# Performance work log

Measured on AMD Instinct MI355X. Metric: run time of the kernel, lower is better.

The kernel has to match this reference:

```python
import jax, jax.numpy as jnp
import numpy as np

EMBED = 2048
MLP = 8192
EPS = 1e-5


def setup_inputs() -> dict:
    key = jax.random.key(0)
    ks = jax.random.split(key, 16)
    s = 0.02
    inp = {
        "x": jax.random.normal(ks[0], (2, 2048, EMBED), dtype=jnp.float32),
        "wq": jax.random.normal(ks[1], (EMBED, EMBED), dtype=jnp.float32) * s,
        "bq": jnp.zeros((EMBED,), jnp.float32),
        "wk": jax.random.normal(ks[2], (EMBED, EMBED), dtype=jnp.float32) * s,
        "bk": jnp.zeros((EMBED,), jnp.float32),
        "wv": jax.random.normal(ks[3], (EMBED, EMBED), dtype=jnp.float32) * s,
        "bv": jnp.zeros((EMBED,), jnp.float32),
        "wd": jax.random.normal(ks[4], (EMBED, EMBED), dtype=jnp.float32) * s,
        "bd": jnp.zeros((EMBED,), jnp.float32),
        "ln_g": jnp.ones((EMBED,), jnp.float32),
        "ln_b": jnp.zeros((EMBED,), jnp.float32),
        "w1": jax.random.normal(ks[5], (MLP, EMBED), dtype=jnp.float32) * s,
        "b1": jnp.zeros((MLP,), jnp.float32),
        "w2": jax.random.normal(ks[6], (EMBED, MLP), dtype=jnp.float32) * s,
        "b2": jnp.zeros((EMBED,), jnp.float32),
    }
    return inp


def _layernorm(x, g, b):
    mu = jnp.mean(x, axis=-1, keepdims=True)
    var = jnp.mean(jnp.square(x - mu), axis=-1, keepdims=True)
    return (x - mu) * jax.lax.rsqrt(var + EPS) * g + b


def reference(x, wq, bq, wk, bk, wv, bv, wd, bd, ln_g, ln_b, w1, b1, w2, b2):
    # Single-head attention; scale uses full embed_dim (rotary_emb.dim == embed_dim).
    q = jnp.einsum("bse,fe->bsf", x, wq) + bq
    k = jnp.einsum("bse,fe->bsf", x, wk) + bk
    v = jnp.einsum("bse,fe->bsf", x, wv) + bv
    scores = jnp.einsum("bqe,bke->bqk", q, k) / jnp.sqrt(jnp.float32(EMBED))
    probs = jax.nn.softmax(scores, axis=-1)
    ctx = jnp.einsum("bqk,bke->bqe", probs, v)
    attn_out = jnp.einsum("bse,fe->bsf", ctx, wd) + bd
    # residual (dropout is identity in eval mode)
    h = x + attn_out
    h = _layernorm(h, ln_g, ln_b)
    mlp = jnp.einsum("bse,fe->bsf", h, w1) + b1
    mlp = jax.nn.gelu(mlp, approximate=False)
    mlp = jnp.einsum("bsf,ef->bse", mlp, w2) + b2
    return h + mlp
```

## Files before the change

### kernel.cpp

```cpp
#include <hip/hip_runtime.h>
#include <math.h>


#define SEQ 2048
#define EMB 2048
#define MLPD 8192

typedef __attribute__((ext_vector_type(8))) short short8;
typedef __attribute__((ext_vector_type(4))) float floatx4;
typedef unsigned short ushort;

__device__ __forceinline__ short f2bf(float f) {
  union { float f; unsigned u; } v; v.f = f;
  unsigned r = v.u + 0x7FFFu + ((v.u >> 16) & 1u);
  return (short)(r >> 16);
}
__device__ __forceinline__ float bf2f(ushort u) {
  union { unsigned u; float f; } v; v.u = ((unsigned)u) << 16;
  return v.f;
}

__device__ __forceinline__ void gload16(const ushort* g, ushort* l) {
  __builtin_amdgcn_global_load_lds(
      (__attribute__((address_space(1))) void*)g,
      (__attribute__((address_space(3))) void*)(unsigned)(unsigned long)l,
      16, 0, 0);
}

enum { EPI_QKV = 0, EPI_SCORES = 1, EPI_PV = 2, EPI_GELU = 4,
       EPI_VT = 5, EPI_SBF16 = 6 };

template<int EPI>
__global__ __launch_bounds__(512, 2)
void gemm256(const ushort* __restrict__ A, const ushort* __restrict__ B,
             const float* __restrict__ bias, void* __restrict__ Cp,
             int N, int K, int lda, int ldb, int ldc,
             long sA, long sB, long sC, float scale)
{
  extern __shared__ ushort lds[];
  const int t = threadIdx.x;
  const int lane = t & 63, w = t >> 6;
  const int wm = w >> 2, wn = w & 3;
  const long bm = (long)blockIdx.y * 256;
  const long bn = (long)blockIdx.x * 256;
  A += (long)blockIdx.z * sA;
  B += (long)blockIdx.z * sB;

  const int srow = (w << 3) + (lane >> 3);
  const int gcol = (lane & 7) ^ ((lane >> 3) & 7);
  const ushort* Ab = A + (bm + srow) * (long)lda + gcol * 8;
  const ushort* Bb = B + (bn + srow) * (long)ldb + gcol * 8;
  ushort* lw = lds + (w << 9);

#define STG_A0(LOFF, KK) do { gload16(Ab + (KK), lw + (LOFF)); \
    gload16(Ab + 64L * lda + (KK), lw + (LOFF) + 4096); } while (0)
#define STG_A1(LOFF, KK) do { gload16(Ab + 128L * lda + (KK), lw + (LOFF)); \
    gload16(Ab + 192L * lda + (KK), lw + (LOFF) + 4096); } while (0)
#define STG_B0(LOFF, KK) do { gload16(Bb + (KK), lw + (LOFF)); \
    gload16(Bb + 64L * ldb + (KK), lw + (LOFF) + 4096); } while (0)
#define STG_B1(LOFF, KK) do { gload16(Bb + 128L * ldb + (KK), lw + (LOFF)); \
    gload16(Bb + 192L * ldb + (KK), lw + (LOFF) + 4096); } while (0)

  const int l15 = lane & 15, q = lane >> 4, swz = l15 & 7;
  const int kx0 = (q ^ swz) << 3;
  const int kx1 = ((4 + q) ^ swz) << 3;
  const int arow = (wm << 13) + l15 * 64;
  const int brow = 16384 + ((wn >> 1) << 13) + ((wn & 1) << 12) + l15 * 64;

  floatx4 acc[8][4];
#pragma unroll
  for (int m = 0; m < 8; ++m)
#pragma unroll
    for (int n = 0; n < 4; ++n) acc[m][n] = (floatx4)0.0f;

  short8 A0[4], A1[4], B0[4], B1[4];

#define LDS8(IDX) (*(const short8*)&lds[IDX])
#define RD_ALK0(CB) do { _Pragma("unroll") for (int mf = 0; mf < 4; ++mf) \
    A0[mf] = LDS8((CB) + arow + mf * 1024 + kx0); } while (0)
#define RD_ALK1(CB) do { _Pragma("unroll") for (int mf = 0; mf < 4; ++mf) \
    A1[mf] = LDS8((CB) + arow + mf * 1024 + kx1); } while (0)
#define RD_AHK0(CB) do { _Pragma("unroll") for (int mf = 0; mf < 4; ++mf) \
    A0[mf] = LDS8((CB) + arow + (4 + mf) * 1024 + kx0); } while (0)
#define RD_AHK1(CB) do { _Pragma("unroll") for (int mf = 0; mf < 4; ++mf) \
    A1[mf] = LDS8((CB) + arow + (4 + mf) * 1024 + kx1); } while (0)
#define RD_BK0(CB) do { _Pragma("unroll") for (int nf = 0; nf < 4; ++nf) \
    B0[nf] = LDS8((CB) + brow + nf * 1024 + kx0); } while (0)
#define RD_BK1(CB) do { _Pragma("unroll") for (int nf = 0; nf < 4; ++nf) \
    B1[nf] = LDS8((CB) + brow + nf * 1024 + kx1); } while (0)

#define MMA16(MO, AX, BX) do {                                            \
    __builtin_amdgcn_s_setprio(1);                                        \
    _Pragma("unroll") for (int mf = 0; mf < 4; ++mf)                      \
      _Pragma("unroll") for (int nf = 0; nf < 4; ++nf)                    \
        acc[(MO)+mf][nf] = __builtin_amdgcn_mfma_f32_16x16x32_bf16(       \
            AX[mf], BX[nf], acc[(MO)+mf][nf], 0, 0, 0);                   \
    __builtin_amdgcn_s_setprio(0);                                        \
  } while (0)

#define BARR() __builtin_amdgcn_s_barrier()
#define VMC4  asm volatile("s_waitcnt vmcnt(4)" ::: "memory")

#define KTILE(CB, NB, K1, K2) do {                                        \
    RD_ALK0(CB); RD_BK0(CB); STG_A0((NB) + 0, K1);                        \
    MMA16(0, A0, B0); BARR();                                             \
    RD_ALK1(CB); RD_BK1(CB); STG_A1((NB) + 8192, K1);                     \
    MMA16(0, A1, B1); BARR();                                             \
    RD_AHK0(CB); STG_B0((CB) + 16384, K2);                                \
    MMA16(4, A0, B0); BARR();                                             \
    RD_AHK1(CB); STG_B1((CB) + 24576, K2);                                \
    MMA16(4, A1, B1); VMC4; BARR();                                       \
  } while (0)

  STG_A0(0, 0);              STG_A1(8192, 0);
  STG_B0(16384, 0);          STG_B1(24576, 0);
  {
    const int k1p = (K > 64) ? 64 : 0;
    STG_B0(32768 + 16384, k1p);
    STG_B1(32768 + 24576, k1p);
  }
  asm volatile("s_waitcnt vmcnt(4)" ::: "memory");
  BARR();

  const int NT = K >> 6;
  for (int kt = 0; kt < NT; kt += 2) {
    const int k1 = ((kt + 1 < NT) ? kt + 1 : NT - 1) << 6;
    const int k2 = ((kt + 2 < NT) ? kt + 2 : NT - 1) << 6;
    const int k3 = ((kt + 3 < NT) ? kt + 3 : NT - 1) << 6;
    KTILE(0,     32768, k1, k2);
    KTILE(32768, 0,     k2, k3);
  }
  asm volatile("s_waitcnt vmcnt(0)" ::: "memory");
#undef KTILE
#undef MMA16
#undef RD_ALK0
#undef RD_ALK1
#undef RD_AHK0
#undef RD_AHK1
#undef RD_BK0
#undef RD_BK1
#undef LDS8
#undef STG_A0
#undef STG_A1
#undef STG_B0
#undef STG_B1

  const int lq = lane >> 4;
#pragma unroll
  for (int mf = 0; mf < 8; ++mf) {
#pragma unroll
    for (int nf = 0; nf < 4; ++nf) {
#pragma unroll
      for (int i = 0; i < 4; ++i) {
        const long r = bm + wm * 128 + mf * 16 + lq * 4 + i;
        const long c = bn + wn * 64 + nf * 16 + l15;
        float val = acc[mf][nf][i];
        if constexpr (EPI == EPI_QKV) {
          val += bias[c];
          ((ushort*)Cp)[r * (long)ldc + c] = (ushort)f2bf(val);
        } else if constexpr (EPI == EPI_SCORES) {
          ((float*)Cp)[(long)blockIdx.z * sC + r * (long)ldc + c] = val * scale;
        } else {
          val += bias[c];
          float g = 0.5f * val * (1.0f + erff(val * 0.70710678118f));
          ((ushort*)Cp)[r * (long)ldc + c] = (ushort)f2bf(g);
        }
      }
    }
  }
}

template<int EPI>
__global__ __launch_bounds__(256)
void gemm_bt(const ushort* __restrict__ A, const ushort* __restrict__ B,
             const float* __restrict__ bias, void* __restrict__ Cp,
             int N, int K, int lda, int ldb, int ldc,
             long sA, long sB, long sC, float scale)
{
  __shared__ ushort As[128 * 32];
  __shared__ ushort Bs[128 * 32];

  const int t = threadIdx.x;
  const int lane = t & 63, wid = t >> 6;
  const int wm = wid >> 1, wn = wid & 1;
  const long bm = (long)blockIdx.y * 128;
  const long bn = (long)blockIdx.x * 128;
  A += (long)blockIdx.z * sA;
  B += (long)blockIdx.z * sB;

  const int srow = (wid << 5) + (lane >> 2);
  const int scol = (lane & 3) << 3;
  const ushort* a0 = A + (bm + srow) * (long)lda + scol;
  const ushort* a1 = a0 + 16L * lda;
  const ushort* b0 = B + (bn + srow) * (long)ldb + scol;
  const ushort* b1 = b0 + 16L * ldb;
  ushort* lA0 = As + (wid << 10);
  ushort* lA1 = lA0 + 512;
  ushort* lB0 = Bs + (wid << 10);
  ushort* lB1 = lB0 + 512;

  floatx4 acc[4][4];
#pragma unroll
  for (int m = 0; m < 4; ++m)
#pragma unroll
    for (int n = 0; n < 4; ++n) acc[m][n] = (floatx4)0.0f;

  const int l15 = lane & 15, kq = (lane >> 4) << 3;
  const int abase = ((wm << 6) + l15) * 32 + kq;
  const int bbase = ((wn << 6) + l15) * 32 + kq;

  for (int kb = 0; kb < K; kb += 32) {
    gload16(a0 + kb, lA0);
    gload16(a1 + kb, lA1);
    gload16(b0 + kb, lB0);
    gload16(b1 + kb, lB1);
    __syncthreads();

    short8 a[4], b[4];
#pragma unroll
    for (int m = 0; m < 4; ++m)
      a[m] = *reinterpret_cast<const short8*>(&As[abase + m * (16 * 32)]);
#pragma unroll
    for (int n = 0; n < 4; ++n)
      b[n] = *reinterpret_cast<const short8*>(&Bs[bbase + n * (16 * 32)]);
#pragma unroll
    for (int m = 0; m < 4; ++m)
#pragma unroll
      for (int n = 0; n < 4; ++n)
        acc[m][n] = __builtin_amdgcn_mfma_f32_16x16x32_bf16(a[m], b[n], acc[m][n], 0, 0, 0);
    __syncthreads();
  }

  const int lq = lane >> 4;
#pragma unroll
  for (int m = 0; m < 4; ++m) {
#pragma unroll
    for (int n = 0; n < 4; ++n) {
#pragma unroll
      for (int i = 0; i < 4; ++i) {
        const long r = bm + wm * 64 + m * 16 + lq * 4 + i;
        const long c = bn + wn * 64 + n * 16 + l15;
        float val = acc[m][n][i];
        if constexpr (EPI == EPI_SBF16) {
          ((ushort*)Cp)[(long)blockIdx.z * sC + r * (long)ldc + c] =
              (ushort)f2bf(val * scale);
        } else if constexpr (EPI == EPI_PV) {
          ((ushort*)Cp)[(long)blockIdx.z * sC + r * (long)ldc + c] = (ushort)f2bf(val);
        } else if constexpr (EPI == EPI_VT) {
          val += bias[r];
          ((ushort*)Cp)[(long)blockIdx.z * sC + r * (long)ldc + c] = (ushort)f2bf(val);
        }
      }
    }
  }
}

__global__ __launch_bounds__(256)
void reduce2(const float* __restrict__ p0, const float* __restrict__ p1,
             const float* __restrict__ bias, const float* __restrict__ res,
             float* __restrict__ out)
{
  const long i = ((long)blockIdx.x * 256 + threadIdx.x) * 8;
  const int c = (int)(i & 2047);
  float4 a0 = *(const float4*)(p0 + i),  a1 = *(const float4*)(p0 + i + 4);
  float4 q0 = *(const float4*)(p1 + i),  q1 = *(const float4*)(p1 + i + 4);
  float4 r0 = *(const float4*)(res + i), r1 = *(const float4*)(res + i + 4);
  float4 b0 = *(const float4*)(bias + c), b1 = *(const float4*)(bias + c + 4);
  float4 o0 = {a0.x + q0.x + r0.x + b0.x, a0.y + q0.y + r0.y + b0.y,
               a0.z + q0.z + r0.z + b0.z, a0.w + q0.w + r0.w + b0.w};
  float4 o1 = {a1.x + q1.x + r1.x + b1.x, a1.y + q1.y + r1.y + b1.y,
               a1.z + q1.z + r1.z + b1.z, a1.w + q1.w + r1.w + b1.w};
  *(float4*)(out + i) = o0;
  *(float4*)(out + i + 4) = o1;
}

__global__ __launch_bounds__(256)
void cvt8(const float* __restrict__ s, ushort* __restrict__ d) {
  const long i = ((long)blockIdx.x * 256 + threadIdx.x) * 8;
  float4 a = *reinterpret_cast<const float4*>(s + i);
  float4 b = *reinterpret_cast<const float4*>(s + i + 4);
  short8 v;
  v[0] = f2bf(a.x); v[1] = f2bf(a.y); v[2] = f2bf(a.z); v[3] = f2bf(a.w);
  v[4] = f2bf(b.x); v[5] = f2bf(b.y); v[6] = f2bf(b.z); v[7] = f2bf(b.w);
  *reinterpret_cast<short8*>(d + i) = v;
}

__global__ __launch_bounds__(256)
void concat2(const float* __restrict__ b0, const float* __restrict__ b1,
             float* __restrict__ dst) {
  const int i = blockIdx.x * 256 + threadIdx.x;
  dst[i] = (i < 2048) ? b0[i] : b1[i - 2048];
}

__global__ __launch_bounds__(256)
void softmax_rows(const ushort* __restrict__ S, ushort* __restrict__ P) {
  const long row = blockIdx.x;
  const ushort* src = S + row * 2048;
  const int t = threadIdx.x, lane = t & 63, wid = t >> 6;
  short8 raw = *reinterpret_cast<const short8*>(src + t * 8);
  float v[8];
#pragma unroll
  for (int i = 0; i < 8; ++i) v[i] = bf2f((ushort)raw[i]);
  float m = v[0];
#pragma unroll
  for (int i = 1; i < 8; ++i) m = fmaxf(m, v[i]);
#pragma unroll
  for (int o = 32; o; o >>= 1) m = fmaxf(m, __shfl_xor(m, o));
  __shared__ float rm[4], rs[4];
  if (!lane) rm[wid] = m;
  __syncthreads();
  m = fmaxf(fmaxf(rm[0], rm[1]), fmaxf(rm[2], rm[3]));
  float e[8], s = 0.f;
#pragma unroll
  for (int i = 0; i < 8; ++i) { e[i] = __expf(v[i] - m); s += e[i]; }
#pragma unroll
  for (int o = 32; o; o >>= 1) s += __shfl_xor(s, o);
  if (!lane) rs[wid] = s;
  __syncthreads();
  s = rs[0] + rs[1] + rs[2] + rs[3];
  const float inv = 1.0f / s;
  short8 wv;
#pragma unroll
  for (int i = 0; i < 8; ++i) wv[i] = f2bf(e[i] * inv);
  *reinterpret_cast<short8*>(P + row * 2048 + t * 8) = wv;
}

__global__ __launch_bounds__(256)
void layernorm_fused(const float* __restrict__ p0, const float* __restrict__ p1,
                     const float* __restrict__ bias, const float* __restrict__ res,
                     const float* __restrict__ g, const float* __restrict__ bb,
                     float* __restrict__ H, ushort* __restrict__ Hb) {
  const long row = blockIdx.x;
  const long base = row * 2048;
  const int t = threadIdx.x, lane = t & 63, wid = t >> 6;
  const long i = base + t * 8;
  const int c0 = t * 8;
  float v[8];
  {
    float4 a0 = *(const float4*)(p0 + i),  a1 = *(const float4*)(p0 + i + 4);
    float4 q0 = *(const float4*)(p1 + i),  q1 = *(const float4*)(p1 + i + 4);
    float4 r0 = *(const float4*)(res + i), r1 = *(const float4*)(res + i + 4);
    float4 b0 = *(const float4*)(bias + c0), b1 = *(const float4*)(bias + c0 + 4);
    v[0] = a0.x + q0.x + r0.x + b0.x; v[1] = a0.y + q0.y + r0.y + b0.y;
    v[2] = a0.z + q0.z + r0.z + b0.z; v[3] = a0.w + q0.w + r0.w + b0.w;
    v[4] = a1.x + q1.x + r1.x + b1.x; v[5] = a1.y + q1.y + r1.y + b1.y;
    v[6] = a1.z + q1.z + r1.z + b1.z; v[7] = a1.w + q1.w + r1.w + b1.w;
  }
  float s = 0.f, ss = 0.f;
#pragma unroll
  for (int i2 = 0; i2 < 8; ++i2) { s += v[i2]; ss += v[i2] * v[i2]; }
#pragma unroll
  for (int o = 32; o; o >>= 1) { s += __shfl_xor(s, o); ss += __shfl_xor(ss, o); }
  __shared__ float r1s[4], r2s[4];
  if (!lane) { r1s[wid] = s; r2s[wid] = ss; }
  __syncthreads();
  s = r1s[0] + r1s[1] + r1s[2] + r1s[3];
  ss = r2s[0] + r2s[1] + r2s[2] + r2s[3];
  const float mu = s * (1.0f / 2048.0f);
  const float var = ss * (1.0f / 2048.0f) - mu * mu;
  const float inv = rsqrtf(var + 1e-5f);
  float o0[8];
  short8 wv;
#pragma unroll
  for (int i2 = 0; i2 < 8; ++i2) {
    const int c = c0 + i2;
    o0[i2] = (v[i2] - mu) * inv * g[c] + bb[c];
    wv[i2] = f2bf(o0[i2]);
  }
  float4 w0 = {o0[0], o0[1], o0[2], o0[3]}, w1 = {o0[4], o0[5], o0[6], o0[7]};
  *reinterpret_cast<float4*>(H + i) = w0;
  *reinterpret_cast<float4*>(H + i + 4) = w1;
  *reinterpret_cast<short8*>(Hb + i) = wv;
}

extern "C" void kernel_launch(void* const* d_in, const int* in_sizes, int n_in,
                              void* d_out, int out_size, void* d_ws, size_t ws_size,
                              hipStream_t stream) {
  const float* x    = (const float*)d_in[0];
  const float* wq   = (const float*)d_in[1];
  const float* bq   = (const float*)d_in[2];
  const float* wk   = (const float*)d_in[3];
  const float* bk   = (const float*)d_in[4];
  const float* wv   = (const float*)d_in[5];
  const float* bv   = (const float*)d_in[6];
  const float* wd   = (const float*)d_in[7];
  const float* bd   = (const float*)d_in[8];
  const float* ln_g = (const float*)d_in[9];
  const float* ln_b = (const float*)d_in[10];
  const float* w1   = (const float*)d_in[11];
  const float* b1   = (const float*)d_in[12];
  const float* w2   = (const float*)d_in[13];
  const float* b2   = (const float*)d_in[14];
  float* out = (float*)d_out;

  (void)hipFuncSetAttribute((const void*)&gemm256<EPI_QKV>,
      hipFuncAttributeMaxDynamicSharedMemorySize, 131072);
  (void)hipFuncSetAttribute((const void*)&gemm256<EPI_GELU>,
      hipFuncAttributeMaxDynamicSharedMemorySize, 131072);
  (void)hipFuncSetAttribute((const void*)&gemm256<EPI_SCORES>,
      hipFuncAttributeMaxDynamicSharedMemorySize, 131072);

  char* p = (char*)d_ws;
  const size_t MB = 1048576;
  ushort* wdb    = (ushort*)(p + 0 * MB);
  ushort* w1b    = (ushort*)(p + 8 * MB);
  ushort* w2b    = (ushort*)(p + 40 * MB);
  float*  bqk    = (float*) (p + 72 * MB);
  ushort* xb     = (ushort*)(p + 73 * MB);
  ushort* probs  = xb;
  ushort* qk     = (ushort*)(p + 89 * MB);
  ushort* wqkb   = (ushort*)(p + 121 * MB);
  ushort* vT     = (ushort*)(p + 121 * MB);
  ushort* wvb    = (ushort*)(p + 137 * MB);
  ushort* scoresb= (ushort*)(p + 137 * MB);
  float*  partA  = (float*) (p + 89 * MB);
  ushort* mlpb   = (ushort*)(p + 89 * MB);
  float*  h      = (float*) (p + 153 * MB);
  ushort* hb     = (ushort*)(p + 185 * MB);
  ushort* ctx    = (ushort*)(p + 201 * MB);
  float*  partM0 = (float*) (p + 0 * MB);
  float*  partM1 = (float*) (p + 201 * MB);

  const dim3 blk(256), blk512(512);
  const long SQ = (long)SEQ * SEQ;

  cvt8<<<4096, blk, 0, stream>>>(x, xb);
  cvt8<<<2048, blk, 0, stream>>>(wq, wqkb);
  cvt8<<<2048, blk, 0, stream>>>(wk, wqkb + 4194304);
  cvt8<<<2048, blk, 0, stream>>>(wv, wvb);
  cvt8<<<2048, blk, 0, stream>>>(wd, wdb);
  cvt8<<<8192, blk, 0, stream>>>(w1, w1b);
  cvt8<<<8192, blk, 0, stream>>>(w2, w2b);
  concat2<<<16, blk, 0, stream>>>(bq, bk, bqk);

  gemm256<EPI_QKV><<<dim3(16, 16, 1), blk512, 131072, stream>>>(
      xb, wqkb, bqk, qk, 4096, 2048, 2048, 2048, 4096, 0, 0, 0, 1.f);

  gemm_bt<EPI_VT><<<dim3(16, 16, 2), blk, 0, stream>>>(
      wvb, xb, bv, vT, 2048, 2048, 2048, 2048, 2048,
      0, SQ, SQ, 1.f);

  gemm_bt<EPI_SBF16><<<dim3(16, 16, 2), blk, 0, stream>>>(
      qk, qk + 2048, nullptr, scoresb, 2048, 2048, 4096, 4096, 2048,
      2048L * 4096, 2048L * 4096, SQ, 0.022097086912079608f);

  softmax_rows<<<dim3(4096), blk, 0, stream>>>(scoresb, probs);

  gemm_bt<EPI_PV><<<dim3(16, 16, 2), blk, 0, stream>>>(
      probs, vT, nullptr, ctx, 2048, 2048, 2048, 2048, 2048,
      SQ, SQ, SQ, 1.f);

  gemm256<EPI_SCORES><<<dim3(8, 16, 2), blk512, 131072, stream>>>(
      ctx, wdb, nullptr, partA, 2048, 1024, 2048, 2048, 2048,
      1024, 1024, 8388608, 1.f);

  layernorm_fused<<<4096, blk, 0, stream>>>(
      partA, partA + 8388608, bd, x, ln_g, ln_b, h, hb);

  gemm256<EPI_GELU><<<dim3(32, 16, 1), blk512, 131072, stream>>>(
      hb, w1b, b1, mlpb, 8192, 2048, 2048, 2048, 8192, 0, 0, 0, 1.f);

  gemm256<EPI_SCORES><<<dim3(8, 16, 2), blk512, 131072, stream>>>(
      mlpb, w2b, nullptr, partM0, 2048, 4096, 8192, 8192, 2048,
      4096, 4096, (long)(201 * MB / 4), 1.f);
  reduce2<<<4096, blk, 0, stream>>>(partM0, partM1, b2, h, out);
}
```

Before: 659.3 us.

## Double GEMM K-tile to 64 with XOR-swizzled LDS layout and MFMA priority

The bf16 GEMM kernel now stages a 128x64 K-slice per iteration instead of 128x32. This halves the number of barrier pairs and loop iterations. The LDS layout uses an XOR swizzle on 16-byte columns, applied at global load time, so that fragment reads avoid bank conflicts. MFMA blocks are wrapped in s_setprio to favour the compute wave. In exchange, LDS use per block doubles and more registers are live, which could lower occupancy.

```diff
diff --git a/kernel.cpp b/kernel.cpp
--- a/kernel.cpp
+++ b/kernel.cpp
@@ -177,8 +177,8 @@
              int N, int K, int lda, int ldb, int ldc,
              long sA, long sB, long sC, float scale)
 {
-  __shared__ ushort As[128 * 32];
-  __shared__ ushort Bs[128 * 32];
+  __shared__ ushort As[128 * 64];
+  __shared__ ushort Bs[128 * 64];
 
   const int t = threadIdx.x;
   const int lane = t & 63, wid = t >> 6;
@@ -188,16 +188,12 @@
   A += (long)blockIdx.z * sA;
   B += (long)blockIdx.z * sB;
 
-  const int srow = (wid << 5) + (lane >> 2);
-  const int scol = (lane & 3) << 3;
-  const ushort* a0 = A + (bm + srow) * (long)lda + scol;
-  const ushort* a1 = a0 + 16L * lda;
-  const ushort* b0 = B + (bn + srow) * (long)ldb + scol;
-  const ushort* b1 = b0 + 16L * ldb;
-  ushort* lA0 = As + (wid << 10);
-  ushort* lA1 = lA0 + 512;
-  ushort* lB0 = Bs + (wid << 10);
-  ushort* lB1 = lB0 + 512;
+  const int srow = (wid << 3) + (lane >> 3);
+  const int gcol = (lane & 7) ^ ((lane >> 3) & 7);
+  const ushort* a0 = A + (bm + srow) * (long)lda + gcol * 8;
+  const ushort* b0 = B + (bn + srow) * (long)ldb + gcol * 8;
+  ushort* lA = As + (wid << 9);
+  ushort* lB = Bs + (wid << 9);
 
   floatx4 acc[4][4];
 #pragma unroll
@@ -205,29 +201,40 @@
 #pragma unroll
     for (int n = 0; n < 4; ++n) acc[m][n] = (floatx4)0.0f;
 
-  const int l15 = lane & 15, kq = (lane >> 4) << 3;
-  const int abase = ((wm << 6) + l15) * 32 + kq;
-  const int bbase = ((wn << 6) + l15) * 32 + kq;
-
-  for (int kb = 0; kb < K; kb += 32) {
-    gload16(a0 + kb, lA0);
-    gload16(a1 + kb, lA1);
-    gload16(b0 + kb, lB0);
-    gload16(b1 + kb, lB1);
+  const int l15 = lane & 15, q = lane >> 4, swz = l15 & 7;
+  const int kx0 = (q ^ swz) << 3;
+  const int kx1 = ((4 + q) ^ swz) << 3;
+  const int abase = ((wm << 6) + l15) * 64;
+  const int bbase = ((wn << 6) + l15) * 64;
+
+  for (int kb = 0; kb < K; kb += 64) {
+#pragma unroll
+    for (int i = 0; i < 4; ++i) {
+      gload16(a0 + (32L * i) * lda + kb, lA + i * 2048);
+      gload16(b0 + (32L * i) * ldb + kb, lB + i * 2048);
+    }
     __syncthreads();
 
-    short8 a[4], b[4];
+    short8 a0r[4], a1r[4], b0r[4], b1r[4];
+#pragma unroll
+    for (int m = 0; m < 4; ++m) {
+      a0r[m] = *reinterpret_cast<const short8*>(&As[abase + m * 1024 + kx0]);
+      a1r[m] = *reinterpret_cast<const short8*>(&As[abase + m * 1024 + kx1]);
+    }
+#pragma unroll
+    for (int n = 0; n < 4; ++n) {
+      b0r[n] = *reinterpret_cast<const short8*>(&Bs[bbase + n * 1024 + kx0]);
+      b1r[n] = *reinterpret_cast<const short8*>(&Bs[bbase + n * 1024 + kx1]);
+    }
+    __builtin_amdgcn_s_setprio(1);
 #pragma unroll
     for (int m = 0; m < 4; ++m)
-      a[m] = *reinterpret_cast<const short8*>(&As[abase + m * (16 * 32)]);
-#pragma unroll
-    for (int n = 0; n < 4; ++n)
-      b[n] = *reinterpret_cast<const short8*>(&Bs[bbase + n * (16 * 32)]);
-#pragma unroll
-    for (int m = 0; m < 4; ++m)
-#pragma unroll
-      for (int n = 0; n < 4; ++n)
-        acc[m][n] = __builtin_amdgcn_mfma_f32_16x16x32_bf16(a[m], b[n], acc[m][n], 0, 0, 0);
+#pragma unroll
+      for (int n = 0; n < 4; ++n) {
+        acc[m][n] = __builtin_amdgcn_mfma_f32_16x16x32_bf16(a0r[m], b0r[n], acc[m][n], 0, 0, 0);
+        acc[m][n] = __builtin_amdgcn_mfma_f32_16x16x32_bf16(a1r[m], b1r[n], acc[m][n], 0, 0, 0);
+      }
+    __builtin_amdgcn_s_setprio(0);
     __syncthreads();
   }
 
```

Result: faster. 625.8 us (-5.1%).
